# Performance work log

Hardware: AMD Instinct MI355X
Metric: run time of the kernel (lower is better)

The kernel has to match this reference:

```python
import jax, jax.numpy as jnp
import numpy as np

IH, IW = 48, 48           # img_size
C = 256                   # inp == oup
NH, HD = 8, 32            # num_heads, head_dims; inner_dim = 256
HID = 4 * C               # MLP hidden
N = IH * IW               # window size (seq len) = 2304
SCALE = (C // NH) ** -0.5 # (inp_dims // num_heads) ** -0.5
EPS = 1e-5


def _relative_position_index():
    coords = np.stack(np.meshgrid(np.arange(IH), np.arange(IW), indexing='ij'))
    cf = coords.reshape(2, -1)
    rel = (cf[:, :, None] - cf[:, None, :]).transpose(1, 2, 0)
    rel[:, :, 0] += IH - 1
    rel[:, :, 1] += IW - 1
    rel[:, :, 0] *= 2 * IW - 1
    return jnp.asarray(rel.sum(-1).astype(np.int32))  # [N, N]


def setup_inputs() -> dict:
    key = jax.random.key(0)
    ks = jax.random.split(key, 12)
    s = 0.02
    return {
        'x': jax.random.normal(ks[0], (1, IH, IW, C), jnp.float32),
        'gamma1': jnp.ones((C,), jnp.float32),
        'beta1': jnp.zeros((C,), jnp.float32),
        'w_qkv': jax.random.normal(ks[1], (C, 3 * NH * HD), jnp.float32) * s,
        'w_proj': jax.random.normal(ks[2], (NH * HD, C), jnp.float32) * s,
        'b_proj': jnp.zeros((C,), jnp.float32),
        'bias_table': jax.random.normal(ks[3], ((2 * IH - 1) * (2 * IW - 1), NH), jnp.float32) * s,
        'gamma2': jnp.ones((C,), jnp.float32),
        'beta2': jnp.zeros((C,), jnp.float32),
        'w_fc1': jax.random.normal(ks[4], (C, HID), jnp.float32) * s,
        'b_fc1': jnp.zeros((HID,), jnp.float32),
        'w_fc2': jax.random.normal(ks[5], (HID, C), jnp.float32) * s,
        'b_fc2': jnp.zeros((C,), jnp.float32),
        'rel_idx': _relative_position_index(),
    }


def _layernorm(x, g, b):
    mu = jnp.mean(x, axis=-1, keepdims=True)
    var = jnp.mean(jnp.square(x - mu), axis=-1, keepdims=True)
    return (x - mu) * jax.lax.rsqrt(var + EPS) * g + b


def reference(x, gamma1, beta1, w_qkv, w_proj, b_proj, bias_table,
              gamma2, beta2, w_fc1, b_fc1, w_fc2, b_fc2, rel_idx):
    shortcut = x                                   # [1, IH, IW, C]
    t = x.reshape(1, N, C)
    t = _layernorm(t, gamma1, beta1)

    # qkv: [1, N, 3*NH*HD] -> q, k, v each [1, NH, N, HD]
    qkv = (t @ w_qkv).reshape(1, N, 3, NH, HD).transpose(2, 0, 3, 1, 4)
    q, k, v = qkv[0], qkv[1], qkv[2]
    q = q * SCALE

    attn = jnp.einsum('bhnd,bhmd->bhnm', q, k)     # [1, NH, N, N]
    # relative position bias: gather table rows by index -> [NH, N, N]
    bias = bias_table[rel_idx.reshape(-1)].reshape(N, N, NH).transpose(2, 0, 1)
    attn = jax.nn.softmax(attn + bias[None], axis=-1)

    o = jnp.einsum('bhnm,bhmd->bhnd', attn, v)     # [1, NH, N, HD]
    o = o.transpose(0, 2, 1, 3).reshape(1, N, NH * HD)
    o = o @ w_proj + b_proj                        # [1, N, C]

    x = shortcut + o.reshape(1, IH, IW, C)
    shortcut = x

    t = _layernorm(x.reshape(1, N, C), gamma2, beta2)
    t = jax.nn.gelu(t @ w_fc1 + b_fc1, approximate=False) @ w_fc2 + b_fc2
    return shortcut + t.reshape(1, IH, IW, C)
```

## Files before the change

### kernel.cpp

```cpp
#include <hip/hip_runtime.h>
#include <hip/hip_bf16.h>
#include <math.h>

#define IH 48
#define IW 48
#define NN 2304
#define CC 256
#define NH 8
#define HD 32
#define HID 1024
#define NBIAS 9025
#define SCALE 0.17677669529663687f
#define LN_EPS 1e-5f

typedef __attribute__((ext_vector_type(8))) short bf16x8;
typedef __attribute__((ext_vector_type(4))) float f32x4;

__device__ __forceinline__ short f2b(float f) {
    __hip_bfloat16 h = __float2bfloat16(f);
    short s; __builtin_memcpy(&s, &h, 2); return s;
}
__device__ __forceinline__ float b2f(short s) {
    __hip_bfloat16 h; __builtin_memcpy(&h, &s, 2); return __bfloat162float(h);
}

__global__ void prep_kernel(const float* __restrict__ x, const float* __restrict__ g,
                            const float* __restrict__ b, short* __restrict__ t1,
                            const float* __restrict__ w_qkv, const float* __restrict__ w_proj,
                            const float* __restrict__ w_fc1, const float* __restrict__ w_fc2,
                            const float* __restrict__ bt,
                            short* __restrict__ o_qkv, short* __restrict__ o_proj,
                            short* __restrict__ o_fc1, short* __restrict__ o_fc2,
                            short* __restrict__ o_bias)
{
    const int bid = blockIdx.x, tid = threadIdx.x;
    if (bid < NN) {
        __shared__ float red[8];
        float v = x[bid * CC + tid];
        float s = v, s2 = v * v;
        #pragma unroll
        for (int off = 32; off > 0; off >>= 1) {
            s  += __shfl_xor(s, off);
            s2 += __shfl_xor(s2, off);
        }
        const int wid = tid >> 6;
        if ((tid & 63) == 0) { red[wid * 2] = s; red[wid * 2 + 1] = s2; }
        __syncthreads();
        float tot  = red[0] + red[2] + red[4] + red[6];
        float tot2 = red[1] + red[3] + red[5] + red[7];
        float mu   = tot * (1.0f / CC);
        float var  = tot2 * (1.0f / CC) - mu * mu;
        float rstd = rsqrtf(var + LN_EPS);
        t1[bid * CC + tid] = f2b((v - mu) * rstd * g[tid] + b[tid]);
        return;
    }
    const int stride = (gridDim.x - NN) * 256;
    for (int i = (bid - NN) * 256 + tid; i < 858632; i += stride) {
        int j = i;
        if (j < 196608)            { int n = j >> 8,  k = j & 255;  o_qkv [j] = f2b(w_qkv [k * 768  + n]); }
        else if ((j -= 196608) < 65536)  { int n = j >> 8,  k = j & 255;  o_proj[j] = f2b(w_proj[k * 256  + n]); }
        else if ((j -= 65536)  < 262144) { int n = j >> 8,  k = j & 255;  o_fc1 [j] = f2b(w_fc1 [k * 1024 + n]); }
        else if ((j -= 262144) < 262144) { int n = j >> 10, k = j & 1023; o_fc2 [j] = f2b(w_fc2 [k * 256  + n]); }
        else { j -= 262144; int h = j / NBIAS, idx = j - h * NBIAS; o_bias[j] = f2b(bt[idx * NH + h]); }
    }
}

__global__ void ln_kernel(const float* __restrict__ x,
                          const float* __restrict__ g,
                          const float* __restrict__ b,
                          short* __restrict__ out)
{
    __shared__ float red[8];
    const int row = blockIdx.x, tid = threadIdx.x;
    float v = x[row * CC + tid];
    float s = v, s2 = v * v;
    #pragma unroll
    for (int off = 32; off > 0; off >>= 1) {
        s  += __shfl_xor(s, off);
        s2 += __shfl_xor(s2, off);
    }
    const int wid = tid >> 6;
    if ((tid & 63) == 0) { red[wid * 2] = s; red[wid * 2 + 1] = s2; }
    __syncthreads();
    float tot  = red[0] + red[2] + red[4] + red[6];
    float tot2 = red[1] + red[3] + red[5] + red[7];
    float mu   = tot * (1.0f / CC);
    float var  = tot2 * (1.0f / CC) - mu * mu;
    float rstd = rsqrtf(var + LN_EPS);
    out[row * CC + tid] = f2b((v - mu) * rstd * g[tid] + b[tid]);
}

#define GSTRIDE 72
template<int K>
__device__ __forceinline__ void mfma_gemm_core(const short* __restrict__ A,
                                               const short* __restrict__ BT,
                                               int m0, int n0, f32x4 acc[4],
                                               short* lds)
{
    short* As = lds;
    short* Bs = lds + 64 * GSTRIDE;
    const int tid  = threadIdx.x;
    const int w    = tid >> 6, lane = tid & 63;
    const int quad = lane >> 4, l15 = lane & 15;
    const int sr = tid >> 2;
    const int sc = (tid & 3) * 16;
    #pragma unroll
    for (int c = 0; c < 4; ++c) acc[c] = (f32x4){0.f, 0.f, 0.f, 0.f};

    const short* Ap = &A [(m0 + sr) * K + sc];
    const short* Bp = &BT[(n0 + sr) * K + sc];
    bf16x8 ra0 = *(const bf16x8*)Ap,       ra1 = *(const bf16x8*)(Ap + 8);
    bf16x8 rb0 = *(const bf16x8*)Bp,       rb1 = *(const bf16x8*)(Bp + 8);

    for (int k0 = 0; k0 < K; k0 += 64) {
        __syncthreads();
        *(bf16x8*)&As[sr * GSTRIDE + sc]     = ra0;
        *(bf16x8*)&As[sr * GSTRIDE + sc + 8] = ra1;
        *(bf16x8*)&Bs[sr * GSTRIDE + sc]     = rb0;
        *(bf16x8*)&Bs[sr * GSTRIDE + sc + 8] = rb1;
        if (k0 + 64 < K) {
            ra0 = *(const bf16x8*)(Ap + k0 + 64);
            ra1 = *(const bf16x8*)(Ap + k0 + 72);
            rb0 = *(const bf16x8*)(Bp + k0 + 64);
            rb1 = *(const bf16x8*)(Bp + k0 + 72);
        }
        __syncthreads();
        #pragma unroll
        for (int s = 0; s < 2; ++s) {
            bf16x8 a = *(const bf16x8*)&As[(w * 16 + l15) * GSTRIDE + s * 32 + quad * 8];
            #pragma unroll
            for (int c = 0; c < 4; ++c) {
                bf16x8 b = *(const bf16x8*)&Bs[(c * 16 + l15) * GSTRIDE + s * 32 + quad * 8];
                acc[c] = __builtin_amdgcn_mfma_f32_16x16x32_bf16(a, b, acc[c], 0, 0, 0);
            }
        }
    }
}

__global__ void qkv_kernel(const short* __restrict__ t1, const short* __restrict__ wT,
                           short* __restrict__ qb, short* __restrict__ kb,
                           short* __restrict__ vT)
{
    __shared__ short lds[2 * 64 * GSTRIDE];
    f32x4 acc[4];
    const int m0 = blockIdx.y * 64, n0 = blockIdx.x * 64;
    mfma_gemm_core<256>(t1, wT, m0, n0, acc, lds);
    const int lane = threadIdx.x & 63, w = threadIdx.x >> 6;
    const int quad = lane >> 4, l15 = lane & 15;
    #pragma unroll
    for (int c = 0; c < 4; ++c) {
        int col = n0 + c * 16 + l15;
        int three = col >> 8, rem = col & 255;
        int h = rem >> 5, d = rem & 31;
        #pragma unroll
        for (int r = 0; r < 4; ++r) {
            int row = m0 + w * 16 + quad * 4 + r;
            float v = acc[c][r];
            if (three == 0)      qb[(h * NN + row) * HD + d] = f2b(v * SCALE);
            else if (three == 1) kb[(h * NN + row) * HD + d] = f2b(v);
            else                 vT[(h * HD + d) * NN + row] = f2b(v);
        }
    }
}

#define PSTRIDE 40
__global__ __launch_bounds__(512) void attn_kernel(
        const short* __restrict__ qb, const short* __restrict__ kb,
        const short* __restrict__ vT, const short* __restrict__ biasT,
        short* __restrict__ o)
{
    __shared__ float Ored[8][16][33];
    __shared__ float lred[8][16];
    __shared__ short sbuf[8][16 * PSTRIDE];
    const int w = threadIdx.x >> 6, lane = threadIdx.x & 63;
    const int quad = lane >> 4, l15 = lane & 15;
    const int h = blockIdx.x / 144, q0 = (blockIdx.x % 144) * 16;
    const int t0 = w * 288;
    short* sb = &sbuf[w][0];
    const short* bt = &biasT[h * NBIAS];

    bf16x8 qf = *(const bf16x8*)&qb[(h * NN + q0 + l15) * HD + quad * 8];

    int base[4];
    #pragma unroll
    for (int r = 0; r < 4; ++r) {
        int row = q0 + quad * 4 + r;
        int qi = row / IW, qj = row % IW;
        base[r] = (qi + 47) * 95 + (qj + 47);
    }

    f32x4 O0 = (f32x4){0.f,0.f,0.f,0.f}, O1 = (f32x4){0.f,0.f,0.f,0.f};
    float lp[4] = {0.f, 0.f, 0.f, 0.f};
    const f32x4 zero = (f32x4){0.f,0.f,0.f,0.f};

    for (int c = 0; c < 9; ++c) {
        const int t = t0 + c * 32;
        bf16x8 k0f = *(const bf16x8*)&kb[(h * NN + t      + l15) * HD + quad * 8];
        bf16x8 k1f = *(const bf16x8*)&kb[(h * NN + t + 16 + l15) * HD + quad * 8];
        f32x4 s0 = __builtin_amdgcn_mfma_f32_16x16x32_bf16(qf, k0f, zero, 0, 0, 0);
        f32x4 s1 = __builtin_amdgcn_mfma_f32_16x16x32_bf16(qf, k1f, zero, 0, 0, 0);
        bf16x8 v0 = *(const bf16x8*)&vT[(h * HD + l15)      * NN + t + quad * 8];
        bf16x8 v1 = *(const bf16x8*)&vT[(h * HD + 16 + l15) * NN + t + quad * 8];

        int key0 = t + l15, key1 = t + 16 + l15;
        int boff0 = -((key0 / IW) * 95 + key0 % IW);
        int boff1 = -((key1 / IW) * 95 + key1 % IW);

        #pragma unroll
        for (int r = 0; r < 4; ++r) {
            float p0 = __expf(s0[r] + b2f(bt[base[r] + boff0]));
            float p1 = __expf(s1[r] + b2f(bt[base[r] + boff1]));
            lp[r] += p0 + p1;
            sb[(quad * 4 + r) * PSTRIDE + l15]      = f2b(p0);
            sb[(quad * 4 + r) * PSTRIDE + 16 + l15] = f2b(p1);
        }
        asm volatile("s_waitcnt lgkmcnt(0)" ::: "memory");
        bf16x8 pa = *(const bf16x8*)&sb[l15 * PSTRIDE + quad * 8];
        O0 = __builtin_amdgcn_mfma_f32_16x16x32_bf16(pa, v0, O0, 0, 0, 0);
        O1 = __builtin_amdgcn_mfma_f32_16x16x32_bf16(pa, v1, O1, 0, 0, 0);
    }

    #pragma unroll
    for (int r = 0; r < 4; ++r) {
        float l = lp[r];
        l += __shfl_xor(l, 1); l += __shfl_xor(l, 2);
        l += __shfl_xor(l, 4); l += __shfl_xor(l, 8);
        if (l15 == 0) lred[w][quad * 4 + r] = l;
        Ored[w][quad * 4 + r][l15]      = O0[r];
        Ored[w][quad * 4 + r][16 + l15] = O1[r];
    }
    __syncthreads();
    {
        int rr  = 2 * w + (lane >> 5);
        int col = lane & 31;
        float s = 0.f, l = 0.f;
        #pragma unroll
        for (int p = 0; p < 8; ++p) { s += Ored[p][rr][col]; l += lred[p][rr]; }
        o[(q0 + rr) * CC + h * HD + col] = f2b(s / l);
    }
}

__global__ void proj_kernel(const short* __restrict__ o, const short* __restrict__ wT,
                            const float* __restrict__ bias, const float* __restrict__ x_in,
                            float* __restrict__ x2)
{
    __shared__ short lds[2 * 64 * GSTRIDE];
    f32x4 acc[4];
    const int m0 = blockIdx.y * 64, n0 = blockIdx.x * 64;
    mfma_gemm_core<256>(o, wT, m0, n0, acc, lds);
    const int lane = threadIdx.x & 63, w = threadIdx.x >> 6;
    const int quad = lane >> 4, l15 = lane & 15;
    #pragma unroll
    for (int c = 0; c < 4; ++c) {
        int col = n0 + c * 16 + l15;
        #pragma unroll
        for (int r = 0; r < 4; ++r) {
            int row = m0 + w * 16 + quad * 4 + r;
            x2[row * CC + col] = acc[c][r] + bias[col] + x_in[row * CC + col];
        }
    }
}

__global__ void fc1_kernel(const short* __restrict__ t2, const short* __restrict__ wT,
                           const float* __restrict__ bias, short* __restrict__ h1)
{
    __shared__ short lds[2 * 64 * GSTRIDE];
    f32x4 acc[4];
    const int m0 = blockIdx.y * 64, n0 = blockIdx.x * 64;
    mfma_gemm_core<256>(t2, wT, m0, n0, acc, lds);
    const int lane = threadIdx.x & 63, w = threadIdx.x >> 6;
    const int quad = lane >> 4, l15 = lane & 15;
    #pragma unroll
    for (int c = 0; c < 4; ++c) {
        int col = n0 + c * 16 + l15;
        #pragma unroll
        for (int r = 0; r < 4; ++r) {
            int row = m0 + w * 16 + quad * 4 + r;
            float v = acc[c][r] + bias[col];
            float ge = 0.5f * v * (1.0f + erff(v * 0.7071067811865476f));
            h1[row * HID + col] = f2b(ge);
        }
    }
}

__global__ void fc2_kernel(const short* __restrict__ h1, const short* __restrict__ wT,
                           const float* __restrict__ bias, const float* __restrict__ x2,
                           float* __restrict__ out)
{
    __shared__ short lds[2 * 64 * GSTRIDE];
    f32x4 acc[4];
    const int m0 = blockIdx.y * 64, n0 = blockIdx.x * 64;
    mfma_gemm_core<1024>(h1, wT, m0, n0, acc, lds);
    const int lane = threadIdx.x & 63, w = threadIdx.x >> 6;
    const int quad = lane >> 4, l15 = lane & 15;
    #pragma unroll
    for (int c = 0; c < 4; ++c) {
        int col = n0 + c * 16 + l15;
        #pragma unroll
        for (int r = 0; r < 4; ++r) {
            int row = m0 + w * 16 + quad * 4 + r;
            out[row * CC + col] = acc[c][r] + bias[col] + x2[row * CC + col];
        }
    }
}

extern "C" void kernel_launch(void* const* d_in, const int* in_sizes, int n_in,
                              void* d_out, int out_size, void* d_ws, size_t ws_size,
                              hipStream_t stream)
{
    const float* x          = (const float*)d_in[0];
    const float* gamma1     = (const float*)d_in[1];
    const float* beta1      = (const float*)d_in[2];
    const float* w_qkv      = (const float*)d_in[3];
    const float* w_proj     = (const float*)d_in[4];
    const float* b_proj     = (const float*)d_in[5];
    const float* bias_table = (const float*)d_in[6];
    const float* gamma2     = (const float*)d_in[7];
    const float* beta2      = (const float*)d_in[8];
    const float* w_fc1      = (const float*)d_in[9];
    const float* b_fc1      = (const float*)d_in[10];
    const float* w_fc2      = (const float*)d_in[11];
    const float* b_fc2      = (const float*)d_in[12];

    short* S = (short*)d_ws;
    const int NC = NN * CC;
    short* t1     = S;
    short* qb     = t1  + NC;
    short* kb     = qb  + NC;
    short* vT     = kb  + NC;
    short* obuf   = vT  + NC;
    short* t2     = obuf+ NC;
    short* h1     = t2  + NC;
    short* wTqkv  = h1  + NN * HID;
    short* wTproj = wTqkv  + 768 * 256;
    short* wTfc1  = wTproj + 256 * 256;
    short* wTfc2  = wTfc1  + 1024 * 256;
    short* biasT  = wTfc2  + 256 * 1024;
    float* x2     = (float*)(biasT + NH * NBIAS + 8);

    prep_kernel<<<NN + 512, 256, 0, stream>>>(x, gamma1, beta1, t1,
                                              w_qkv, w_proj, w_fc1, w_fc2, bias_table,
                                              wTqkv, wTproj, wTfc1, wTfc2, biasT);
    qkv_kernel<<<dim3(12, 36), 256, 0, stream>>>(t1, wTqkv, qb, kb, vT);
    attn_kernel<<<1152, 512, 0, stream>>>(qb, kb, vT, biasT, obuf);
    proj_kernel<<<dim3(4, 36), 256, 0, stream>>>(obuf, wTproj, b_proj, x, x2);
    ln_kernel<<<NN, 256, 0, stream>>>(x2, gamma2, beta2, t2);
    fc1_kernel<<<dim3(16, 36), 256, 0, stream>>>(t2, wTfc1, b_fc1, h1);
    fc2_kernel<<<dim3(4, 36), 256, 0, stream>>>(h1, wTfc2, b_fc2, x2,
                                                (float*)d_out);
}
```

Measured before the change: 164.7 us.

## Compute S transposed in registers to drop LDS P round-trip, use exp2

Result: slower. 187.9 us (+14.1%).

```diff
diff --git a/kernel.cpp b/kernel.cpp
--- a/kernel.cpp
+++ b/kernel.cpp
@@ -11,9 +11,11 @@
 #define HID 1024
 #define NBIAS 9025
 #define SCALE 0.17677669529663687f
+#define LOG2E 1.4426950408889634f
 #define LN_EPS 1e-5f
 
 typedef __attribute__((ext_vector_type(8))) short bf16x8;
+typedef __attribute__((ext_vector_type(4))) short bf16x4;
 typedef __attribute__((ext_vector_type(4))) float f32x4;
 
 __device__ __forceinline__ short f2b(float f) {
@@ -22,6 +24,13 @@
 }
 __device__ __forceinline__ float b2f(short s) {
     __hip_bfloat16 h; __builtin_memcpy(&h, &s, 2); return __bfloat162float(h);
+}
+__device__ __forceinline__ float fast_exp2(float x) {
+#if __has_builtin(__builtin_amdgcn_exp2f)
+    return __builtin_amdgcn_exp2f(x);
+#else
+    return exp2f(x);
+#endif
 }
 
 __global__ void prep_kernel(const float* __restrict__ x, const float* __restrict__ g,
@@ -61,7 +70,7 @@
         else if ((j -= 196608) < 65536)  { int n = j >> 8,  k = j & 255;  o_proj[j] = f2b(w_proj[k * 256  + n]); }
         else if ((j -= 65536)  < 262144) { int n = j >> 8,  k = j & 255;  o_fc1 [j] = f2b(w_fc1 [k * 1024 + n]); }
         else if ((j -= 262144) < 262144) { int n = j >> 10, k = j & 1023; o_fc2 [j] = f2b(w_fc2 [k * 256  + n]); }
-        else { j -= 262144; int h = j / NBIAS, idx = j - h * NBIAS; o_bias[j] = f2b(bt[idx * NH + h]); }
+        else { j -= 262144; int h = j / NBIAS, idx = j - h * NBIAS; o_bias[j] = f2b(bt[idx * NH + h] * LOG2E); }
     }
 }
 
@@ -156,87 +165,89 @@
         for (int r = 0; r < 4; ++r) {
             int row = m0 + w * 16 + quad * 4 + r;
             float v = acc[c][r];
-            if (three == 0)      qb[(h * NN + row) * HD + d] = f2b(v * SCALE);
+            if (three == 0)      qb[(h * NN + row) * HD + d] = f2b(v * (SCALE * LOG2E));
             else if (three == 1) kb[(h * NN + row) * HD + d] = f2b(v);
             else                 vT[(h * HD + d) * NN + row] = f2b(v);
         }
     }
 }
 
-#define PSTRIDE 40
-__global__ __launch_bounds__(512) void attn_kernel(
+__global__ __launch_bounds__(256) void attn_kernel(
         const short* __restrict__ qb, const short* __restrict__ kb,
         const short* __restrict__ vT, const short* __restrict__ biasT,
         short* __restrict__ o)
 {
-    __shared__ float Ored[8][16][33];
-    __shared__ float lred[8][16];
-    __shared__ short sbuf[8][16 * PSTRIDE];
+    __shared__ float Ored[4][16][33];
+    __shared__ float lred[4][16];
     const int w = threadIdx.x >> 6, lane = threadIdx.x & 63;
     const int quad = lane >> 4, l15 = lane & 15;
     const int h = blockIdx.x / 144, q0 = (blockIdx.x % 144) * 16;
-    const int t0 = w * 288;
-    short* sb = &sbuf[w][0];
+    const int t0 = w * 576;
     const short* bt = &biasT[h * NBIAS];
 
     bf16x8 qf = *(const bf16x8*)&qb[(h * NN + q0 + l15) * HD + quad * 8];
 
-    int base[4];
-    #pragma unroll
-    for (int r = 0; r < 4; ++r) {
-        int row = q0 + quad * 4 + r;
-        int qi = row / IW, qj = row % IW;
-        base[r] = (qi + 47) * 95 + (qj + 47);
-    }
+    const int qi = q0 / IW, qj = (q0 % IW) + l15;
+    const int qbase = (qi + 47) * 95 + (qj + 47);
 
     f32x4 O0 = (f32x4){0.f,0.f,0.f,0.f}, O1 = (f32x4){0.f,0.f,0.f,0.f};
-    float lp[4] = {0.f, 0.f, 0.f, 0.f};
+    float lp = 0.f;
     const f32x4 zero = (f32x4){0.f,0.f,0.f,0.f};
 
-    for (int c = 0; c < 9; ++c) {
+    for (int c = 0; c < 18; ++c) {
         const int t = t0 + c * 32;
         bf16x8 k0f = *(const bf16x8*)&kb[(h * NN + t      + l15) * HD + quad * 8];
         bf16x8 k1f = *(const bf16x8*)&kb[(h * NN + t + 16 + l15) * HD + quad * 8];
-        f32x4 s0 = __builtin_amdgcn_mfma_f32_16x16x32_bf16(qf, k0f, zero, 0, 0, 0);
-        f32x4 s1 = __builtin_amdgcn_mfma_f32_16x16x32_bf16(qf, k1f, zero, 0, 0, 0);
-        bf16x8 v0 = *(const bf16x8*)&vT[(h * HD + l15)      * NN + t + quad * 8];
-        bf16x8 v1 = *(const bf16x8*)&vT[(h * HD + 16 + l15) * NN + t + quad * 8];
-
-        int key0 = t + l15, key1 = t + 16 + l15;
-        int boff0 = -((key0 / IW) * 95 + key0 % IW);
-        int boff1 = -((key1 / IW) * 95 + key1 % IW);
-
-        #pragma unroll
-        for (int r = 0; r < 4; ++r) {
-            float p0 = __expf(s0[r] + b2f(bt[base[r] + boff0]));
-            float p1 = __expf(s1[r] + b2f(bt[base[r] + boff1]));
-            lp[r] += p0 + p1;
-            sb[(quad * 4 + r) * PSTRIDE + l15]      = f2b(p0);
-            sb[(quad * 4 + r) * PSTRIDE + 16 + l15] = f2b(p1);
-        }
-        asm volatile("s_waitcnt lgkmcnt(0)" ::: "memory");
-        bf16x8 pa = *(const bf16x8*)&sb[l15 * PSTRIDE + quad * 8];
+        const short* vp0 = &vT[(h * HD + l15)      * NN + t + quad * 4];
+        const short* vp1 = &vT[(h * HD + 16 + l15) * NN + t + quad * 4];
+        bf16x4 va0 = *(const bf16x4*)vp0, vb0 = *(const bf16x4*)(vp0 + 16);
+        bf16x4 va1 = *(const bf16x4*)vp1, vb1 = *(const bf16x4*)(vp1 + 16);
+
+        f32x4 s0 = __builtin_amdgcn_mfma_f32_16x16x32_bf16(k0f, qf, zero, 0, 0, 0);
+        f32x4 s1 = __builtin_amdgcn_mfma_f32_16x16x32_bf16(k1f, qf, zero, 0, 0, 0);
+
+        const int kA = t + quad * 4;
+        const int kiA = kA / IW, kjA = kA % IW;
+        const int kB = kA + 16;
+        const int kiB = kB / IW, kjB = kB % IW;
+        const short* pA = bt + (qbase - (kiA * 95 + kjA));
+        const short* pB = bt + (qbase - (kiB * 95 + kjB));
+
+        float p[8];
+        #pragma unroll
+        for (int r = 0; r < 4; ++r) {
+            p[r]     = fast_exp2(s0[r] + b2f(pA[-r]));
+            p[4 + r] = fast_exp2(s1[r] + b2f(pB[-r]));
+        }
+        #pragma unroll
+        for (int r = 0; r < 8; ++r) lp += p[r];
+        bf16x8 pa = (bf16x8){ f2b(p[0]), f2b(p[1]), f2b(p[2]), f2b(p[3]),
+                              f2b(p[4]), f2b(p[5]), f2b(p[6]), f2b(p[7]) };
+        bf16x8 v0 = (bf16x8){ va0[0], va0[1], va0[2], va0[3],
+                              vb0[0], vb0[1], vb0[2], vb0[3] };
+        bf16x8 v1 = (bf16x8){ va1[0], va1[1], va1[2], va1[3],
+                              vb1[0], vb1[1], vb1[2], vb1[3] };
         O0 = __builtin_amdgcn_mfma_f32_16x16x32_bf16(pa, v0, O0, 0, 0, 0);
         O1 = __builtin_amdgcn_mfma_f32_16x16x32_bf16(pa, v1, O1, 0, 0, 0);
     }
 
+    lp += __shfl_xor(lp, 16);
+    lp += __shfl_xor(lp, 32);
+    if (quad == 0) lred[w][l15] = lp;
     #pragma unroll
     for (int r = 0; r < 4; ++r) {
-        float l = lp[r];
-        l += __shfl_xor(l, 1); l += __shfl_xor(l, 2);
-        l += __shfl_xor(l, 4); l += __shfl_xor(l, 8);
-        if (l15 == 0) lred[w][quad * 4 + r] = l;
         Ored[w][quad * 4 + r][l15]      = O0[r];
         Ored[w][quad * 4 + r][16 + l15] = O1[r];
     }
     __syncthreads();
     {
-        int rr  = 2 * w + (lane >> 5);
-        int col = lane & 31;
-        float s = 0.f, l = 0.f;
-        #pragma unroll
-        for (int p = 0; p < 8; ++p) { s += Ored[p][rr][col]; l += lred[p][rr]; }
-        o[(q0 + rr) * CC + h * HD + col] = f2b(s / l);
+        const int col = threadIdx.x & 31;
+        for (int rr = threadIdx.x >> 5; rr < 16; rr += 8) {
+            float s = 0.f, l = 0.f;
+            #pragma unroll
+            for (int pw = 0; pw < 4; ++pw) { s += Ored[pw][rr][col]; l += lred[pw][rr]; }
+            o[(q0 + rr) * CC + h * HD + col] = f2b(s / l);
+        }
     }
 }
 
@@ -342,7 +353,7 @@
                                               w_qkv, w_proj, w_fc1, w_fc2, bias_table,
                                               wTqkv, wTproj, wTfc1, wTfc2, biasT);
     qkv_kernel<<<dim3(12, 36), 256, 0, stream>>>(t1, wTqkv, qb, kb, vT);
-    attn_kernel<<<1152, 512, 0, stream>>>(qb, kb, vT, biasT, obuf);
+    attn_kernel<<<1152, 256, 0, stream>>>(qb, kb, vT, biasT, obuf);
     proj_kernel<<<dim3(4, 36), 256, 0, stream>>>(obuf, wTproj, b_proj, x, x2);
     ln_kernel<<<NN, 256, 0, stream>>>(x2, gamma2, beta2, t2);
     fc1_kernel<<<dim3(16, 36), 256, 0, stream>>>(t2, wTfc1, b_fc1, h1);
```
